# Performance work log

Measured on AMD Instinct MI355X. Metric: run time of the kernel, lower is better.

The kernel has to match this reference:

```python
import jax, jax.numpy as jnp
import numpy as np


def setup_inputs() -> dict:
    key = jax.random.key(0)
    kq, kk, kv = jax.random.split(key, 3)
    B, H, S, D = 2, 16, 2048, 64
    q = jax.random.normal(kq, (B, H, S, D), dtype=jnp.float32)
    k = jax.random.normal(kk, (B, H, S, D), dtype=jnp.float32)
    v = jax.random.normal(kv, (B, H, S, D), dtype=jnp.float32)
    return {"q": q, "k": k, "v": v}


def reference(q, k, v):
    # Tiled attention without online softmax computes the same math as
    # standard scaled dot-product attention (non-causal).
    D = q.shape[-1]
    scale = 1.0 / jnp.sqrt(jnp.asarray(D, dtype=q.dtype))
    # scores: [B, H, Sq, Sk]
    scores = jnp.einsum("bhqd,bhkd->bhqk", q, k) * scale
    attn = jax.nn.softmax(scores, axis=-1)
    out = jnp.einsum("bhqk,bhkd->bhqd", attn, v)
    return out
```

## Files before the change

kernel.cpp:

```cpp
#include <hip/hip_runtime.h>
#include <hip/hip_bf16.h>
#include <stdint.h>


#define B_ 2
#define H_ 16
#define S_ 2048
#define D_ 64
#define BH_ (B_ * H_)
#define QBLK 128
#define KVBLK 64
#define NKV (S_ / KVBLK)
#define NPER (NKV / 2)

typedef __bf16 bf16_t;
typedef bf16_t bf16x8 __attribute__((ext_vector_type(8)));
typedef bf16_t bf16x4 __attribute__((ext_vector_type(4)));
typedef float f32x16 __attribute__((ext_vector_type(16)));
typedef uint32_t u32;

__device__ __forceinline__ f32x16 mfma32(bf16x8 a, bf16x8 b, f32x16 c) {
  return __builtin_amdgcn_mfma_f32_32x32x16_bf16(a, b, c, 0, 0, 0);
}

__device__ __forceinline__ u32 cvt_pk_bf16(float lo, float hi) {
  u32 r;
  asm("v_cvt_pk_bf16_f32 %0, %1, %2" : "=v"(r) : "v"(lo), "v"(hi));
  return r;
}

__device__ __forceinline__ void swap32(u32& x, u32& y) {
  asm("v_permlane32_swap_b32 %0, %1" : "+v"(x), "+v"(y));
}

__device__ __forceinline__ void gload_lds16(const bf16_t* g, bf16_t* l) {
  __builtin_amdgcn_global_load_lds(
      (const __attribute__((address_space(1))) unsigned int*)g,
      (__attribute__((address_space(3))) unsigned int*)l, 16, 0, 0);
}

__global__ void convert_k_kernel(const float* __restrict__ k, bf16_t* __restrict__ kb) {
  int i = blockIdx.x * blockDim.x + threadIdx.x;
  float4 x = ((const float4*)k)[i];
  bf16x4 o = { (bf16_t)x.x, (bf16_t)x.y, (bf16_t)x.z, (bf16_t)x.w };
  *(bf16x4*)(kb + (size_t)i * 4) = o;
}

__global__ void transpose_v_kernel(const float* __restrict__ v, bf16_t* __restrict__ vt) {
  __shared__ float tile[64][65];
  int bh = blockIdx.y, kt = blockIdx.x;
  const float* vp = v + ((size_t)bh * S_ + (size_t)kt * 64) * D_;
  int r0 = threadIdx.x >> 4;
  int c4 = (threadIdx.x & 15) * 4;
#pragma unroll
  for (int p = 0; p < 4; ++p) {
    int r = r0 + p * 16;
    float4 x = *(const float4*)(vp + (size_t)r * D_ + c4);
    tile[r][c4 + 0] = x.x; tile[r][c4 + 1] = x.y;
    tile[r][c4 + 2] = x.z; tile[r][c4 + 3] = x.w;
  }
  __syncthreads();
  bf16_t* op = vt + (size_t)bh * D_ * S_ + (size_t)kt * 64;
#pragma unroll
  for (int p = 0; p < 4; ++p) {
    int d = r0 + p * 16;
    bf16x4 o = { (bf16_t)tile[c4 + 0][d], (bf16_t)tile[c4 + 1][d],
                 (bf16_t)tile[c4 + 2][d], (bf16_t)tile[c4 + 3][d] };
    *(bf16x4*)(op + (size_t)d * S_ + c4) = o;
  }
}

__global__ __launch_bounds__(512, 4) void attn_kernel(
    const float* __restrict__ q, const bf16_t* __restrict__ kb,
    const bf16_t* __restrict__ vt, float* __restrict__ out) {
  const int bh = blockIdx.y;
  const int qt = blockIdx.x;
  const int tid = threadIdx.x;
  const int wid = tid >> 6;
  const int lane = tid & 63;
  const int wq = wid & 3;
  const int wkv = wid >> 2;
  const int l31 = lane & 31;
  const int hi = lane >> 5;

  __shared__ __align__(16) char smem[65536];
  bf16_t* kbuf = (bf16_t*)smem;
  bf16_t* vbuf = (bf16_t*)(smem + 32768);
  float* epi = (float*)smem;

  const bf16_t* kp = kb + (size_t)bh * S_ * D_;
  const bf16_t* vp = vt + (size_t)bh * D_ * S_;

  const int srow = tid >> 3;
  const int scol = (tid & 7) ^ (srow & 7);
  const int kofs = srow * D_ + scol * 8;
  const size_t vofs = (size_t)srow * S_ + scol * 8;
  const int ldst = wid * 512;

  const float qscale = 0.125f * 1.4426950408889634f;
  const int qrow = qt * QBLK + wq * 32 + l31;
  const float* qpr = q + ((size_t)bh * S_ + qrow) * D_;
  bf16x8 bq[4];
#pragma unroll
  for (int ks = 0; ks < 4; ++ks) {
    const float* p = qpr + ks * 16 + hi * 8;
    float4 x0 = *(const float4*)(p);
    float4 x1 = *(const float4*)(p + 4);
    bf16x8 a;
    a[0] = (bf16_t)(x0.x * qscale); a[1] = (bf16_t)(x0.y * qscale);
    a[2] = (bf16_t)(x0.z * qscale); a[3] = (bf16_t)(x0.w * qscale);
    a[4] = (bf16_t)(x1.x * qscale); a[5] = (bf16_t)(x1.y * qscale);
    a[6] = (bf16_t)(x1.z * qscale); a[7] = (bf16_t)(x1.w * qscale);
    bq[ks] = a;
  }

  float lsum = 0.f;
  f32x16 o0, o1;
#pragma unroll
  for (int r = 0; r < 16; ++r) { o0[r] = 0.f; o1[r] = 0.f; }

#pragma unroll
  for (int par = 0; par < 2; ++par) {
    gload_lds16(kp + (size_t)par * (KVBLK * D_) + kofs, kbuf + par * 4096 + ldst);
    gload_lds16(vp + (size_t)par * KVBLK + vofs, vbuf + par * 4096 + ldst);
  }
  __syncthreads();

  for (int p = 0; p < NPER; ++p) {
    if (p + 1 < NPER) {
      const int nb = ((p + 1) & 1) * 2;
#pragma unroll
      for (int par = 0; par < 2; ++par) {
        const int t = 2 * p + 2 + par;
        gload_lds16(kp + (size_t)t * (KVBLK * D_) + kofs,
                    kbuf + (nb + par) * 4096 + ldst);
        gload_lds16(vp + (size_t)t * KVBLK + vofs,
                    vbuf + (nb + par) * 4096 + ldst);
      }
    }

    const bf16_t* kt_ = kbuf + ((p & 1) * 2 + wkv) * 4096;
    const bf16_t* vt_ = vbuf + ((p & 1) * 2 + wkv) * 4096;

    u32 w[2][8];
#pragma unroll
    for (int sub = 0; sub < 2; ++sub) {
      f32x16 sv;
#pragma unroll
      for (int r = 0; r < 16; ++r) sv[r] = 0.f;
#pragma unroll
      for (int ks = 0; ks < 4; ++ks) {
        const int row = sub * 32 + l31;
        const int ch = (2 * ks + hi) ^ (row & 7);
        bf16x8 a = *(const bf16x8*)(kt_ + row * D_ + ch * 8);
        sv = mfma32(a, bq[ks], sv);
      }
#pragma unroll
      for (int b = 0; b < 4; ++b) {
        float e0 = __builtin_amdgcn_exp2f(sv[4 * b + 0]);
        float e1 = __builtin_amdgcn_exp2f(sv[4 * b + 1]);
        float e2 = __builtin_amdgcn_exp2f(sv[4 * b + 2]);
        float e3 = __builtin_amdgcn_exp2f(sv[4 * b + 3]);
        lsum += (e0 + e1) + (e2 + e3);
        w[sub][2 * b + 0] = cvt_pk_bf16(e0, e1);
        w[sub][2 * b + 1] = cvt_pk_bf16(e2, e3);
      }
#pragma unroll
      for (int kt2 = 0; kt2 < 2; ++kt2) {
        swap32(w[sub][4 * kt2 + 0], w[sub][4 * kt2 + 2]);
        swap32(w[sub][4 * kt2 + 1], w[sub][4 * kt2 + 3]);
      }
    }

#pragma unroll
    for (int sub = 0; sub < 2; ++sub)
#pragma unroll
      for (int kt2 = 0; kt2 < 2; ++kt2) {
        union { u32 u[4]; bf16x8 v; } pb;
        pb.u[0] = w[sub][4 * kt2 + 0]; pb.u[1] = w[sub][4 * kt2 + 1];
        pb.u[2] = w[sub][4 * kt2 + 2]; pb.u[3] = w[sub][4 * kt2 + 3];
        {
          const int row = l31;
          const int ch = (4 * sub + 2 * kt2 + hi) ^ (row & 7);
          bf16x8 a = *(const bf16x8*)(vt_ + row * KVBLK + ch * 8);
          o0 = mfma32(a, pb.v, o0);
        }
        {
          const int row = 32 + l31;
          const int ch = (4 * sub + 2 * kt2 + hi) ^ (row & 7);
          bf16x8 a = *(const bf16x8*)(vt_ + row * KVBLK + ch * 8);
          o1 = mfma32(a, pb.v, o1);
        }
      }

    __syncthreads();
  }

  if (wkv == 1) {
    float* e = epi + ((size_t)wq * 64 + lane) * 33;
#pragma unroll
    for (int r = 0; r < 16; ++r) { e[r] = o0[r]; e[16 + r] = o1[r]; }
    e[32] = lsum;
  }
  __syncthreads();
  if (wkv == 0) {
    const float* e = epi + ((size_t)wq * 64 + lane) * 33;
#pragma unroll
    for (int r = 0; r < 16; ++r) { o0[r] += e[r]; o1[r] += e[16 + r]; }
    lsum += e[32];
    float ltot = lsum + __shfl_xor(lsum, 32, 64);
    float inv = 1.f / ltot;
    float* op = out + ((size_t)bh * S_ + qrow) * D_;
#pragma unroll
    for (int b = 0; b < 4; ++b) {
      float4 w0 = { o0[4 * b + 0] * inv, o0[4 * b + 1] * inv,
                    o0[4 * b + 2] * inv, o0[4 * b + 3] * inv };
      *(float4*)(op + 8 * b + 4 * hi) = w0;
      float4 w1 = { o1[4 * b + 0] * inv, o1[4 * b + 1] * inv,
                    o1[4 * b + 2] * inv, o1[4 * b + 3] * inv };
      *(float4*)(op + 32 + 8 * b + 4 * hi) = w1;
    }
  }
}

extern "C" void kernel_launch(void* const* d_in, const int* in_sizes, int n_in,
                              void* d_out, int out_size, void* d_ws, size_t ws_size,
                              hipStream_t stream) {
  const float* q = (const float*)d_in[0];
  const float* k = (const float*)d_in[1];
  const float* v = (const float*)d_in[2];
  float* out = (float*)d_out;

  bf16_t* kb = (bf16_t*)d_ws;
  bf16_t* vt = kb + (size_t)BH_ * S_ * D_;

  int n4 = (BH_ * S_ * D_) / 4;
  convert_k_kernel<<<n4 / 256, 256, 0, stream>>>(k, kb);
  transpose_v_kernel<<<dim3(S_ / 64, BH_), 256, 0, stream>>>(v, vt);
  attn_kernel<<<dim3(S_ / QBLK, BH_), 512, 0, stream>>>(q, kb, vt, out);
}
```

Baseline: 58.87 us.

## Halve KV stage size so each wave splits one 64-key block, raising occupancy

```diff
diff --git a/kernel.cpp b/kernel.cpp
--- a/kernel.cpp
+++ b/kernel.cpp
@@ -11,7 +11,6 @@
 #define QBLK 128
 #define KVBLK 64
 #define NKV (S_ / KVBLK)
-#define NPER (NKV / 2)
 
 typedef __bf16 bf16_t;
 typedef bf16_t bf16x8 __attribute__((ext_vector_type(8)));
@@ -70,7 +69,7 @@
   }
 }
 
-__global__ __launch_bounds__(512, 4) void attn_kernel(
+__global__ __launch_bounds__(512, 6) void attn_kernel(
     const float* __restrict__ q, const bf16_t* __restrict__ kb,
     const bf16_t* __restrict__ vt, float* __restrict__ out) {
   const int bh = blockIdx.y;
@@ -83,9 +82,9 @@
   const int l31 = lane & 31;
   const int hi = lane >> 5;
 
-  __shared__ __align__(16) char smem[65536];
+  __shared__ __align__(16) char smem[33792];
   bf16_t* kbuf = (bf16_t*)smem;
-  bf16_t* vbuf = (bf16_t*)(smem + 32768);
+  bf16_t* vbuf = (bf16_t*)(smem + 16384);
   float* epi = (float*)smem;
 
   const bf16_t* kp = kb + (size_t)bh * S_ * D_;
@@ -119,79 +118,69 @@
 #pragma unroll
   for (int r = 0; r < 16; ++r) { o0[r] = 0.f; o1[r] = 0.f; }
 
-#pragma unroll
-  for (int par = 0; par < 2; ++par) {
-    gload_lds16(kp + (size_t)par * (KVBLK * D_) + kofs, kbuf + par * 4096 + ldst);
-    gload_lds16(vp + (size_t)par * KVBLK + vofs, vbuf + par * 4096 + ldst);
-  }
+  gload_lds16(kp + kofs, kbuf + ldst);
+  gload_lds16(vp + vofs, vbuf + ldst);
   __syncthreads();
 
-  for (int p = 0; p < NPER; ++p) {
-    if (p + 1 < NPER) {
-      const int nb = ((p + 1) & 1) * 2;
-#pragma unroll
-      for (int par = 0; par < 2; ++par) {
-        const int t = 2 * p + 2 + par;
-        gload_lds16(kp + (size_t)t * (KVBLK * D_) + kofs,
-                    kbuf + (nb + par) * 4096 + ldst);
-        gload_lds16(vp + (size_t)t * KVBLK + vofs,
-                    vbuf + (nb + par) * 4096 + ldst);
-      }
-    }
-
-    const bf16_t* kt_ = kbuf + ((p & 1) * 2 + wkv) * 4096;
-    const bf16_t* vt_ = vbuf + ((p & 1) * 2 + wkv) * 4096;
-
-    u32 w[2][8];
-#pragma unroll
-    for (int sub = 0; sub < 2; ++sub) {
-      f32x16 sv;
-#pragma unroll
-      for (int r = 0; r < 16; ++r) sv[r] = 0.f;
+  for (int p = 0; p < NKV; ++p) {
+    if (p + 1 < NKV) {
+      const int t = p + 1;
+      const int nb = (t & 1) * 4096;
+      gload_lds16(kp + (size_t)t * (KVBLK * D_) + kofs, kbuf + nb + ldst);
+      gload_lds16(vp + (size_t)t * KVBLK + vofs, vbuf + nb + ldst);
+    }
+
+    const bf16_t* kt_ = kbuf + (p & 1) * 4096;
+    const bf16_t* vt_ = vbuf + (p & 1) * 4096;
+
+    f32x16 sv;
+#pragma unroll
+    for (int r = 0; r < 16; ++r) sv[r] = 0.f;
+    {
+      const int row = wkv * 32 + l31;
 #pragma unroll
       for (int ks = 0; ks < 4; ++ks) {
-        const int row = sub * 32 + l31;
         const int ch = (2 * ks + hi) ^ (row & 7);
         bf16x8 a = *(const bf16x8*)(kt_ + row * D_ + ch * 8);
         sv = mfma32(a, bq[ks], sv);
       }
-#pragma unroll
-      for (int b = 0; b < 4; ++b) {
-        float e0 = __builtin_amdgcn_exp2f(sv[4 * b + 0]);
-        float e1 = __builtin_amdgcn_exp2f(sv[4 * b + 1]);
-        float e2 = __builtin_amdgcn_exp2f(sv[4 * b + 2]);
-        float e3 = __builtin_amdgcn_exp2f(sv[4 * b + 3]);
-        lsum += (e0 + e1) + (e2 + e3);
-        w[sub][2 * b + 0] = cvt_pk_bf16(e0, e1);
-        w[sub][2 * b + 1] = cvt_pk_bf16(e2, e3);
+    }
+
+    u32 w[8];
+#pragma unroll
+    for (int b = 0; b < 4; ++b) {
+      float e0 = __builtin_amdgcn_exp2f(sv[4 * b + 0]);
+      float e1 = __builtin_amdgcn_exp2f(sv[4 * b + 1]);
+      float e2 = __builtin_amdgcn_exp2f(sv[4 * b + 2]);
+      float e3 = __builtin_amdgcn_exp2f(sv[4 * b + 3]);
+      lsum += (e0 + e1) + (e2 + e3);
+      w[2 * b + 0] = cvt_pk_bf16(e0, e1);
+      w[2 * b + 1] = cvt_pk_bf16(e2, e3);
+    }
+#pragma unroll
+    for (int kt2 = 0; kt2 < 2; ++kt2) {
+      swap32(w[4 * kt2 + 0], w[4 * kt2 + 2]);
+      swap32(w[4 * kt2 + 1], w[4 * kt2 + 3]);
+    }
+
+#pragma unroll
+    for (int kt2 = 0; kt2 < 2; ++kt2) {
+      union { u32 u[4]; bf16x8 v; } pb;
+      pb.u[0] = w[4 * kt2 + 0]; pb.u[1] = w[4 * kt2 + 1];
+      pb.u[2] = w[4 * kt2 + 2]; pb.u[3] = w[4 * kt2 + 3];
+      {
+        const int row = l31;
+        const int ch = (wkv * 4 + 2 * kt2 + hi) ^ (row & 7);
+        bf16x8 a = *(const bf16x8*)(vt_ + row * KVBLK + ch * 8);
+        o0 = mfma32(a, pb.v, o0);
       }
-#pragma unroll
-      for (int kt2 = 0; kt2 < 2; ++kt2) {
-        swap32(w[sub][4 * kt2 + 0], w[sub][4 * kt2 + 2]);
-        swap32(w[sub][4 * kt2 + 1], w[sub][4 * kt2 + 3]);
+      {
+        const int row = 32 + l31;
+        const int ch = (wkv * 4 + 2 * kt2 + hi) ^ (row & 7);
+        bf16x8 a = *(const bf16x8*)(vt_ + row * KVBLK + ch * 8);
+        o1 = mfma32(a, pb.v, o1);
       }
     }
-
-#pragma unroll
-    for (int sub = 0; sub < 2; ++sub)
-#pragma unroll
-      for (int kt2 = 0; kt2 < 2; ++kt2) {
-        union { u32 u[4]; bf16x8 v; } pb;
-        pb.u[0] = w[sub][4 * kt2 + 0]; pb.u[1] = w[sub][4 * kt2 + 1];
-        pb.u[2] = w[sub][4 * kt2 + 2]; pb.u[3] = w[sub][4 * kt2 + 3];
-        {
-          const int row = l31;
-          const int ch = (4 * sub + 2 * kt2 + hi) ^ (row & 7);
-          bf16x8 a = *(const bf16x8*)(vt_ + row * KVBLK + ch * 8);
-          o0 = mfma32(a, pb.v, o0);
-        }
-        {
-          const int row = 32 + l31;
-          const int ch = (4 * sub + 2 * kt2 + hi) ^ (row & 7);
-          bf16x8 a = *(const bf16x8*)(vt_ + row * KVBLK + ch * 8);
-          o1 = mfma32(a, pb.v, o1);
-        }
-      }
 
     __syncthreads();
   }
```

New measurement: 79.48 us. 35.0% more time.
